# Optimization experiments

Hardware: AMD Instinct MI355X
Metric: run time of the kernel (lower is better)

The kernel has to match this reference:

```python
import math
import jax, jax.numpy as jnp
import numpy as np
from jax import lax

B, H, W, C1, D, NH = 32, 28, 28, 64, 256, 8
KS, RATIO = 9, 0.0005
NEG = -1.0e9


def setup_inputs() -> dict:
    key = jax.random.key(0)
    ks = jax.random.split(key, 6)
    x = jax.random.normal(ks[0], (B, 1, H, W), jnp.float32)
    conv_w = jax.random.normal(ks[1], (C1, 1, KS, KS), jnp.float32) * 0.05
    channel_embed = jax.random.normal(ks[2], (C1, D), jnp.float32)
    in_proj_w = jax.random.normal(ks[3], (3 * D, D), jnp.float32) * (1.0 / math.sqrt(D))
    in_proj_b = jnp.zeros((3 * D,), jnp.float32)
    out_proj_w = jax.random.normal(ks[4], (D, D), jnp.float32) * (1.0 / math.sqrt(D))
    out_proj_b = jnp.zeros((D,), jnp.float32)
    return {"x": x, "conv_w": conv_w, "channel_embed": channel_embed,
            "in_proj_w": in_proj_w, "in_proj_b": in_proj_b,
            "out_proj_w": out_proj_w, "out_proj_b": out_proj_b}


def _pos_encoding_2d(h, w, dim):
    # even dims: sin(y * div), odd dims: cos(x * div)  (matches torch broadcast)
    div = jnp.exp(jnp.arange(0, dim, 2, dtype=jnp.float32) * (-math.log(10000.0) / dim))
    pe_even = jnp.sin(jnp.arange(h, dtype=jnp.float32)[:, None] * div)  # (h, dim/2)
    pe_odd = jnp.cos(jnp.arange(w, dtype=jnp.float32)[:, None] * div)   # (w, dim/2)
    pe = jnp.zeros((h, w, dim), jnp.float32)
    pe = pe.at[..., 0::2].set(jnp.broadcast_to(pe_even[:, None, :], (h, w, dim // 2)))
    pe = pe.at[..., 1::2].set(jnp.broadcast_to(pe_odd[None, :, :], (h, w, dim // 2)))
    return pe


def reference(x, conv_w, channel_embed, in_proj_w, in_proj_b, out_proj_w, out_proj_b):
    pad = KS // 2
    A = jax.nn.relu(lax.conv_general_dilated(
        x, conv_w, (1, 1), [(pad, pad), (pad, pad)],
        dimension_numbers=("NCHW", "OIHW", "NCHW")))  # (B, C1, H, W)

    # global top-k threshold (kthvalue equivalent)
    total = A.size
    k = max(1, int(math.ceil(RATIO * total)))
    if k >= total:
        mask_global = jnp.ones_like(A, dtype=bool)
    else:
        vals, _ = lax.top_k(A.reshape(-1), k)
        mask_global = A >= vals[-1]
    A_g = A * mask_global.astype(A.dtype)

    v = jnp.transpose(A_g, (0, 2, 3, 1))  # (B, H, W, C1)
    nz = v > 0
    count = nz.sum(axis=-1)  # (B, H, W)

    top2_vals, top2_idx = lax.top_k(v, 2)  # (B,H,W,2)
    cidx = jnp.arange(C1)
    sel2 = (cidx == top2_idx[..., 0:1]) | (cidx == top2_idx[..., 1:2])
    idx_single = jnp.argmax(jnp.where(nz, v, -jnp.inf), axis=-1)
    sel1 = cidx == idx_single[..., None]

    logits = jnp.where((count >= 2)[..., None] & sel2, v, NEG)
    logits = jnp.where((count == 1)[..., None] & sel1, v, logits)
    sparse_weights = jax.nn.softmax(logits, axis=-1)
    sparse_weights = jnp.where((count == 0)[..., None], 0.0, sparse_weights)

    loc_emb = jnp.einsum("bhwc,cd->bhwd", sparse_weights, channel_embed)
    loc_emb = loc_emb + _pos_encoding_2d(H, W, D)[None]
    seq = loc_emb.reshape(B, H * W, D)

    # torch nn.MultiheadAttention (batch_first, self-attn)
    qkv = seq @ in_proj_w.T + in_proj_b  # (B, S, 3D)
    q, kk, vv = jnp.split(qkv, 3, axis=-1)
    hd = D // NH
    def heads(t):
        return t.reshape(B, H * W, NH, hd).transpose(0, 2, 1, 3)  # (B, NH, S, hd)
    q, kk, vv = heads(q), heads(kk), heads(vv)
    scores = jnp.einsum("bnqd,bnkd->bnqk", q, kk) / math.sqrt(hd)
    attn = jax.nn.softmax(scores, axis=-1)
    ctx = jnp.einsum("bnqk,bnkd->bnqd", attn, vv)
    ctx = ctx.transpose(0, 2, 1, 3).reshape(B, H * W, D)
    attn_out = ctx @ out_proj_w.T + out_proj_b
    pooled = attn_out.mean(axis=1)  # (B, D)
    return pooled, sparse_weights, top2_idx
```

## Files before the change

### kernel.cpp

```cpp
#include <hip/hip_runtime.h>
#include <cmath>

#define NB 32
#define C1N 64
#define DIM 256
#define NHEAD 8
#define SEQL 784
#define NA 1605632
#define SEQN 6422528
#define KSEL 803u
#define QK2S (0.17677669529663687f * 1.4426950408889634f)
#define THR2 11.541560f
#define PECOEF (-0.03597789207803197f)

#define AS1 __attribute__((address_space(1)))
#define AS3 __attribute__((address_space(3)))

typedef __attribute__((ext_vector_type(8))) short bf16x8;
typedef __attribute__((ext_vector_type(4))) float f32x4;

__device__ __forceinline__ unsigned short f2b(float f) {
  unsigned u = __float_as_uint(f);
  unsigned r = u + 0x7fffu + ((u >> 16) & 1u);
  return (unsigned short)(r >> 16);
}

__device__ __forceinline__ unsigned cvt_pk_bf16(float lo, float hi) {
  unsigned r;
  asm("v_cvt_pk_bf16_f32 %0, %1, %2" : "=v"(r) : "v"(lo), "v"(hi));
  return r;
}

__global__ void k_zero(unsigned* __restrict__ p, int n) {
  int i = blockIdx.x * 256 + threadIdx.x;
  if (i < n) p[i] = 0u;
}

__global__ __launch_bounds__(256) void k_cast(const float* __restrict__ ipw,
                                              unsigned short* __restrict__ wb) {
  int i = blockIdx.x * 256 + threadIdx.x;
  wb[i] = f2b(ipw[i]);
}

__global__ __launch_bounds__(256) void k_conv(const float* __restrict__ x,
                                              const float* __restrict__ cw,
                                              float* __restrict__ vbuf) {
  __shared__ __align__(16) float ximg[1296];
  __shared__ float wlds[5184];
  int tid = threadIdx.x;
  int b = blockIdx.x / 7, sblk = blockIdx.x % 7;
  for (int e = tid; e < 1296; e += 256) ximg[e] = 0.f;
  for (int e = tid; e < 5184; e += 256) {
    int c = e / 81, t = e - c * 81;
    wlds[t * 64 + c] = cw[e];
  }
  __syncthreads();
  const float* xb = x + b * 784;
  for (int e = tid; e < 784; e += 256) {
    int row = e / 28, col = e - row * 28;
    ximg[(row + 4) * 36 + col + 4] = xb[e];
  }
  __syncthreads();
  int wv = tid >> 6, lane = tid & 63;
  for (int it = 0; it < 7; ++it) {
    int grp = sblk * 28 + it * 4 + wv;
    int hr = grp / 7, wc0 = (grp % 7) * 4;
    float a0 = 0.f, a1 = 0.f, a2 = 0.f, a3 = 0.f;
    #pragma unroll
    for (int dy = 0; dy < 9; ++dy) {
      const float4* xr4 = (const float4*)&ximg[(hr + dy) * 36 + wc0];
      float4 xa = xr4[0], xbq = xr4[1], xc = xr4[2];
      float xr[12] = {xa.x, xa.y, xa.z, xa.w, xbq.x, xbq.y, xbq.z, xbq.w,
                      xc.x, xc.y, xc.z, xc.w};
      #pragma unroll
      for (int dx = 0; dx < 9; ++dx) {
        float w = wlds[(dy * 9 + dx) * 64 + lane];
        a0 = fmaf(xr[dx + 0], w, a0);
        a1 = fmaf(xr[dx + 1], w, a1);
        a2 = fmaf(xr[dx + 2], w, a2);
        a3 = fmaf(xr[dx + 3], w, a3);
      }
    }
    size_t base = ((size_t)(b * 784 + hr * 28 + wc0)) * 64 + lane;
    vbuf[base +   0] = fmaxf(a0, 0.f);
    vbuf[base +  64] = fmaxf(a1, 0.f);
    vbuf[base + 128] = fmaxf(a2, 0.f);
    vbuf[base + 192] = fmaxf(a3, 0.f);
  }
}

__global__ __launch_bounds__(256) void k_h8(const float* __restrict__ vbuf,
                                            const unsigned* __restrict__ sel,
                                            unsigned* __restrict__ hist8,
                                            int stage) {
  __shared__ unsigned lh[256];
  int tid = threadIdx.x;
  lh[tid] = 0u;
  __syncthreads();
  if (stage == 0 || sel[2] == 0u) {
    unsigned key = (stage == 1) ? sel[0] : 0u;
    const float4* v4 = (const float4*)vbuf;
    int n4 = NA / 4;
    for (int i = blockIdx.x * 256 + tid; i < n4; i += gridDim.x * 256) {
      float4 v = v4[i];
      float vv[4] = {v.x, v.y, v.z, v.w};
      #pragma unroll
      for (int j = 0; j < 4; ++j) {
        if (vv[j] > 0.0f) {
          unsigned bits = __float_as_uint(vv[j]);
          if (stage == 0) atomicAdd(&lh[bits >> 24], 1u);
          else if ((bits >> 24) == key) atomicAdd(&lh[(bits >> 16) & 0xFFu], 1u);
        }
      }
    }
  }
  __syncthreads();
  if (lh[tid] > 0u) atomicAdd(&hist8[tid], lh[tid]);
}

__global__ __launch_bounds__(256) void k_scan8(const unsigned* __restrict__ hist8,
                                               unsigned* __restrict__ sel,
                                               int stage) {
  if (stage == 1 && sel[2]) return;
  __shared__ unsigned ss[256];
  int t = threadIdx.x;
  ss[t] = hist8[t];
  __syncthreads();
  for (int off = 1; off < 256; off <<= 1) {
    unsigned v = (t + off < 256) ? ss[t + off] : 0u;
    __syncthreads();
    ss[t] += v;
    __syncthreads();
  }
  unsigned rem = (stage == 0) ? KSEL : sel[1];
  if (stage == 0 && t == 0 && ss[0] < KSEL) {
    sel[2] = 1u; sel[3] = 0u;
  }
  unsigned S = ss[t];
  unsigned above = (t < 255) ? ss[t + 1] : 0u;
  if (S >= rem && above < rem) {
    if (stage == 0) { sel[0] = (unsigned)t; sel[1] = rem - above; }
    else            { sel[4] = (unsigned)t; sel[5] = rem - above; }
  }
}

__global__ __launch_bounds__(256) void k_h16(const float* __restrict__ vbuf,
                                             const unsigned* __restrict__ sel,
                                             unsigned* __restrict__ hist16) {
  if (sel[2]) return;
  unsigned key16 = (sel[0] << 8) | sel[4];
  const float4* v4 = (const float4*)vbuf;
  int n4 = NA / 4;
  for (int i = blockIdx.x * 256 + threadIdx.x; i < n4; i += gridDim.x * 256) {
    float4 v = v4[i];
    float vv[4] = {v.x, v.y, v.z, v.w};
    #pragma unroll
    for (int j = 0; j < 4; ++j) {
      if (vv[j] > 0.0f) {
        unsigned bits = __float_as_uint(vv[j]);
        if ((bits >> 16) == key16) atomicAdd(&hist16[bits & 0xFFFFu], 1u);
      }
    }
  }
}

__global__ __launch_bounds__(1024) void k_scan16(const unsigned* __restrict__ hist16,
                                                 unsigned* __restrict__ sel) {
  if (sel[2]) return;
  __shared__ unsigned ss[1024];
  int t = threadIdx.x;
  unsigned rem = sel[5];
  unsigned sum = 0;
  for (int i = 0; i < 64; ++i) sum += hist16[t * 64 + i];
  ss[t] = sum;
  __syncthreads();
  for (int off = 1; off < 1024; off <<= 1) {
    unsigned v = (t + off < 1024) ? ss[t + off] : 0u;
    __syncthreads();
    ss[t] += v;
    __syncthreads();
  }
  unsigned S = ss[t];
  unsigned above = (t < 1023) ? ss[t + 1] : 0u;
  if (S >= rem && above < rem) {
    unsigned cum = above;
    for (int bb = t * 64 + 63; bb >= t * 64; --bb) {
      unsigned hb = hist16[bb];
      cum += hb;
      if (cum >= rem) {
        sel[3] = (((sel[0] << 8) | sel[4]) << 16) | (unsigned)bb;
        break;
      }
    }
  }
}

__global__ __launch_bounds__(256) void k_select(const float* __restrict__ vbuf,
                                                const unsigned* __restrict__ sel,
                                                const float* __restrict__ ce,
                                                unsigned short* __restrict__ seqb,
                                                float* __restrict__ out_sw,
                                                float* __restrict__ out_idx) {
  int wid = threadIdx.x >> 6;
  int lane = threadIdx.x & 63;
  int pos = blockIdx.x * 4 + wid;
  int hw = pos % 784;
  int hr = hw / 28;
  int wc = hw % 28;
  float thr = __uint_as_float(sel[3]);
  float a = vbuf[(size_t)pos * 64 + lane];
  float val = (a >= thr) ? a : 0.0f;
  unsigned long long nzm = __ballot(val > 0.0f);
  int count = __popcll(nzm);
  float v1 = val; int i1 = lane;
  #pragma unroll
  for (int off = 32; off > 0; off >>= 1) {
    float ov = __shfl_xor(v1, off);
    int oi = __shfl_xor(i1, off);
    if (ov > v1 || (ov == v1 && oi < i1)) { v1 = ov; i1 = oi; }
  }
  float vx = (lane == i1) ? -INFINITY : val;
  float v2 = vx; int i2 = lane;
  #pragma unroll
  for (int off = 32; off > 0; off >>= 1) {
    float ov = __shfl_xor(v2, off);
    int oi = __shfl_xor(i2, off);
    if (ov > v2 || (ov == v2 && oi < i2)) { v2 = ov; i2 = oi; }
  }
  float w1 = 0.0f, w2 = 0.0f;
  if (count >= 2) {
    float e = __expf(v2 - v1);
    float invd = 1.0f / (1.0f + e);
    w1 = invd; w2 = e * invd;
  } else if (count == 1) {
    w1 = 1.0f;
  }
  float wt = (lane == i1) ? w1 : ((lane == i2) ? w2 : 0.0f);
  out_sw[(size_t)pos * 64 + lane] = wt;
  if (lane < 2) out_idx[pos * 2 + lane] = (float)(lane == 0 ? i1 : i2);
  int d0 = lane * 4;
  float4 c1v = *(const float4*)(ce + (size_t)i1 * 256 + d0);
  float4 c2v = *(const float4*)(ce + (size_t)i2 * 256 + d0);
  float dv0 = __expf((float)d0 * PECOEF);
  float dv2 = __expf((float)(d0 + 2) * PECOEF);
  float ox = w1 * c1v.x + w2 * c2v.x + __sinf((float)hr * dv0);
  float oy = w1 * c1v.y + w2 * c2v.y + __cosf((float)wc * dv0);
  float oz = w1 * c1v.z + w2 * c2v.z + __sinf((float)hr * dv2);
  float ow = w1 * c1v.w + w2 * c2v.w + __cosf((float)wc * dv2);
  ushort4 ob = make_ushort4(f2b(ox), f2b(oy), f2b(oz), f2b(ow));
  *(ushort4*)(seqb + (size_t)pos * 256 + d0) = ob;
}

__global__ __launch_bounds__(256) void k_gemm_lds(const unsigned short* __restrict__ A,
                                                  const unsigned short* __restrict__ W,
                                                  const float* __restrict__ bias,
                                                  unsigned short* __restrict__ C,
                                                  int M, int N, int K) {
  __shared__ __align__(16) unsigned short As[8192];
  __shared__ __align__(16) unsigned short Bs[8192];
  int tid = threadIdx.x;
  int lane = tid & 63, wid = tid >> 6;
  int q = lane & 15, g = lane >> 4;
  int m0 = blockIdx.y * 128, n0 = blockIdx.x * 128;
  int lrow = lane >> 3, s = lane & 7;
  const unsigned short* aSrc = A + (size_t)(m0 + wid * 8 + lrow) * K + (s ^ lrow) * 8;
  const unsigned short* bSrc = W + (size_t)(n0 + wid * 8 + lrow) * K + (s ^ lrow) * 8;
  int dstW = wid * 512;
  int mloc = (wid >> 1) * 64, nloc = (wid & 1) * 64;
  int q7 = q & 7;
  f32x4 acc[4][4];
  #pragma unroll
  for (int i = 0; i < 4; ++i)
    #pragma unroll
    for (int j = 0; j < 4; ++j) acc[i][j] = (f32x4){0.f, 0.f, 0.f, 0.f};
  for (int k0 = 0; k0 < K; k0 += 64) {
    #pragma unroll
    for (int i = 0; i < 4; ++i) {
      __builtin_amdgcn_global_load_lds((const AS1 void*)(aSrc + (size_t)i * 32 * K + k0),
                                       (AS3 void*)(&As[i * 2048 + dstW]), 16, 0, 0);
      __builtin_amdgcn_global_load_lds((const AS1 void*)(bSrc + (size_t)i * 32 * K + k0),
                                       (AS3 void*)(&Bs[i * 2048 + dstW]), 16, 0, 0);
    }
    __syncthreads();
    #pragma unroll
    for (int kk = 0; kk < 2; ++kk) {
      bf16x8 af[4], bf[4];
      #pragma unroll
      for (int i = 0; i < 4; ++i)
        af[i] = *(const bf16x8*)&As[(mloc + i * 16 + q) * 64 + (((kk * 4 + g) ^ q7) * 8)];
      #pragma unroll
      for (int j = 0; j < 4; ++j)
        bf[j] = *(const bf16x8*)&Bs[(nloc + j * 16 + q) * 64 + (((kk * 4 + g) ^ q7) * 8)];
      __builtin_amdgcn_s_setprio(1);
      #pragma unroll
      for (int i = 0; i < 4; ++i)
        #pragma unroll
        for (int j = 0; j < 4; ++j)
          acc[i][j] = __builtin_amdgcn_mfma_f32_16x16x32_bf16(af[i], bf[j], acc[i][j], 0, 0, 0);
      __builtin_amdgcn_s_setprio(0);
    }
    __syncthreads();
  }
  #pragma unroll
  for (int j = 0; j < 4; ++j) {
    int col = n0 + nloc + j * 16 + q;
    float bj = bias[col];
    float qs = (col < 256) ? QK2S : 1.0f;
    #pragma unroll
    for (int i = 0; i < 4; ++i) {
      #pragma unroll
      for (int r = 0; r < 4; ++r) {
        int row = m0 + mloc + i * 16 + g * 4 + r;
        C[(size_t)row * N + col] = f2b((acc[i][j][r] + bj) * qs);
      }
    }
  }
}

__global__ __launch_bounds__(256) void k_vt(const unsigned short* __restrict__ qkv,
                                            unsigned short* __restrict__ Vt) {
  __shared__ unsigned short lds[32][72];
  int k0 = blockIdx.x * 64;
  int bh = blockIdx.y;
  int b = bh >> 3, nh = bh & 7;
  int tid = threadIdx.x;
  int key = tid >> 2;
  int c8 = (tid & 3) * 8;
  int kk = k0 + key;
  ushort4 a = make_ushort4(0, 0, 0, 0), bq = a;
  if (kk < 784) {
    const unsigned short* src = qkv + (size_t)(b * 784 + kk) * 768 + 512 + nh * 32 + c8;
    a  = *(const ushort4*)src;
    bq = *(const ushort4*)(src + 4);
  }
  lds[c8 + 0][key] = a.x;  lds[c8 + 1][key] = a.y;
  lds[c8 + 2][key] = a.z;  lds[c8 + 3][key] = a.w;
  lds[c8 + 4][key] = bq.x; lds[c8 + 5][key] = bq.y;
  lds[c8 + 6][key] = bq.z; lds[c8 + 7][key] = bq.w;
  __syncthreads();
  int d = tid >> 3;
  int kc = (tid & 7) * 8;
  if (k0 + kc < 800) {
    int sb = (kc & 32) + ((kc >> 3) & 3) * 4;
    ushort4 o0 = make_ushort4(lds[d][sb + 0],  lds[d][sb + 1],
                              lds[d][sb + 2],  lds[d][sb + 3]);
    ushort4 o1 = make_ushort4(lds[d][sb + 16], lds[d][sb + 17],
                              lds[d][sb + 18], lds[d][sb + 19]);
    unsigned short* dst = Vt + ((size_t)bh * 32 + d) * 800 + k0 + kc;
    *(ushort4*)dst = o0;
    *(ushort4*)(dst + 4) = o1;
  }
}

__global__ __launch_bounds__(256) void k_attn(const unsigned short* __restrict__ qkv,
                                              const unsigned short* __restrict__ Vt,
                                              unsigned short* __restrict__ ctx) {
  __shared__ __align__(16) unsigned short Kt[2][1024];
  __shared__ __align__(16) unsigned short Vti[2][1024];
  int wid = threadIdx.x >> 6;
  int lane = threadIdx.x & 63;
  int blk = blockIdx.x;
  int wb = (blk & 7) * 416 + (blk >> 3);
  int bh = wb / 13;
  int qb = (wb - bh * 13) * 4 + wid;
  int b = bh >> 3, nh = bh & 7;
  int q = lane & 15, g = lane >> 4;
  bool active = (qb < 49);
  const f32x4 zero4 = {0.f, 0.f, 0.f, 0.f};

  int qrow = b * 784 + (active ? qb * 16 + q : q);
  bf16x8 qf = *(const bf16x8*)(qkv + (size_t)qrow * 768 + nh * 32 + g * 8);
  const unsigned short* kbase = qkv + (size_t)b * 784 * 768 + 256 + nh * 32;
  const unsigned short* vbase = Vt + (size_t)bh * 32 * 800;

  int rit = ((wid & 1) << 4) + (lane >> 2);
  int sG = (lane & 3) ^ ((rit + (rit >> 2)) & 3);
  bool isK = (wid < 2);
  int ldsoff = ((wid & 1) << 4) * 32;

  int slotr = ((g ^ ((q + (q >> 2)) & 3)) << 3);
  int rowA = q * 32 + slotr;
  int rowB = (16 + q) * 32 + slotr;

  f32x4 acc0 = zero4, acc1 = zero4;
  float m = -INFINITY, lp = 0.f;

#define STAGE(buf, k0v)                                                         \
  {                                                                             \
    if (isK) {                                                                  \
      int key_ = (k0v) + rit; if (key_ > 783) key_ = 783;                       \
      __builtin_amdgcn_global_load_lds(                                         \
        (const AS1 void*)(kbase + (size_t)key_ * 768 + sG * 8),                 \
        (AS3 void*)(&Kt[buf][ldsoff]), 16, 0, 0);                               \
    } else {                                                                    \
      __builtin_amdgcn_global_load_lds(                                         \
        (const AS1 void*)(vbase + (size_t)rit * 800 + (k0v) + sG * 8),          \
        (AS3 void*)(&Vti[buf][ldsoff]), 16, 0, 0);                              \
    }                                                                           \
  }

  STAGE(0, 0);
  __syncthreads();

  for (int c = 0; c < 24; ++c) {
    int cur = c & 1;
    STAGE(cur ^ 1, (c + 1) * 32);
    bf16x8 kA = *(const bf16x8*)&Kt[cur][rowA];
    bf16x8 kB = *(const bf16x8*)&Kt[cur][rowB];
    bf16x8 va = *(const bf16x8*)&Vti[cur][rowA];
    bf16x8 vb = *(const bf16x8*)&Vti[cur][rowB];
    __builtin_amdgcn_s_setprio(1);
    f32x4 s0 = __builtin_amdgcn_mfma_f32_16x16x32_bf16(kA, qf, zero4, 0, 0, 0);
    f32x4 s1 = __builtin_amdgcn_mfma_f32_16x16x32_bf16(kB, qf, zero4, 0, 0, 0);
    __builtin_amdgcn_s_setprio(0);
    float pl = fmaxf(fmaxf(fmaxf(s0[0], s0[1]), fmaxf(s0[2], s0[3])),
                     fmaxf(fmaxf(s1[0], s1[1]), fmaxf(s1[2], s1[3])));
    if (!__all(pl <= m + THR2)) {
      float pm = fmaxf(pl, __shfl_xor(pl, 16));
      pm = fmaxf(pm, __shfl_xor(pm, 32));
      float mnew = fmaxf(m, pm);
      float sc = __builtin_amdgcn_exp2f(m - mnew);
      lp *= sc; acc0 *= sc; acc1 *= sc;
      m = mnew;
    }
    float p0[4], p1[4];
    #pragma unroll
    for (int r = 0; r < 4; ++r) {
      p0[r] = __builtin_amdgcn_exp2f(s0[r] - m);
      p1[r] = __builtin_amdgcn_exp2f(s1[r] - m);
    }
    lp += ((p0[0] + p0[1]) + (p0[2] + p0[3])) + ((p1[0] + p1[1]) + (p1[2] + p1[3]));
    union { unsigned u[4]; bf16x8 v; } pu;
    pu.u[0] = cvt_pk_bf16(p0[0], p0[1]);
    pu.u[1] = cvt_pk_bf16(p0[2], p0[3]);
    pu.u[2] = cvt_pk_bf16(p1[0], p1[1]);
    pu.u[3] = cvt_pk_bf16(p1[2], p1[3]);
    __builtin_amdgcn_s_setprio(1);
    acc0 = __builtin_amdgcn_mfma_f32_16x16x32_bf16(va, pu.v, acc0, 0, 0, 0);
    acc1 = __builtin_amdgcn_mfma_f32_16x16x32_bf16(vb, pu.v, acc1, 0, 0, 0);
    __builtin_amdgcn_s_setprio(0);
    __syncthreads();
  }
  {
    bf16x8 kA = *(const bf16x8*)&Kt[0][rowA];
    bf16x8 va = *(const bf16x8*)&Vti[0][rowA];
    bf16x8 vb = *(const bf16x8*)&Vti[0][rowB];
    f32x4 s0 = __builtin_amdgcn_mfma_f32_16x16x32_bf16(kA, qf, zero4, 0, 0, 0);
    float pl = fmaxf(fmaxf(s0[0], s0[1]), fmaxf(s0[2], s0[3]));
    if (!__all(pl <= m + THR2)) {
      float pm = fmaxf(pl, __shfl_xor(pl, 16));
      pm = fmaxf(pm, __shfl_xor(pm, 32));
      float mnew = fmaxf(m, pm);
      float sc = __builtin_amdgcn_exp2f(m - mnew);
      lp *= sc; acc0 *= sc; acc1 *= sc;
      m = mnew;
    }
    float p0[4];
    #pragma unroll
    for (int r = 0; r < 4; ++r) p0[r] = __builtin_amdgcn_exp2f(s0[r] - m);
    lp += (p0[0] + p0[1]) + (p0[2] + p0[3]);
    union { unsigned u[4]; bf16x8 v; } pu;
    pu.u[0] = cvt_pk_bf16(p0[0], p0[1]);
    pu.u[1] = cvt_pk_bf16(p0[2], p0[3]);
    pu.u[2] = 0u;
    pu.u[3] = 0u;
    acc0 = __builtin_amdgcn_mfma_f32_16x16x32_bf16(va, pu.v, acc0, 0, 0, 0);
    acc1 = __builtin_amdgcn_mfma_f32_16x16x32_bf16(vb, pu.v, acc1, 0, 0, 0);
  }
#undef STAGE
  float l = lp + __shfl_xor(lp, 16);
  l += __shfl_xor(l, 32);
  float linv = 1.f / l;
  if (active) {
    unsigned short* cp = ctx + (size_t)(b * 784 + qb * 16 + q) * 256 + nh * 32;
    ushort4 oA = make_ushort4(f2b(acc0[0] * linv), f2b(acc0[1] * linv),
                              f2b(acc0[2] * linv), f2b(acc0[3] * linv));
    ushort4 oB = make_ushort4(f2b(acc1[0] * linv), f2b(acc1[1] * linv),
                              f2b(acc1[2] * linv), f2b(acc1[3] * linv));
    *(ushort4*)(cp + g * 4) = oA;
    *(ushort4*)(cp + 16 + g * 4) = oB;
  }
}

__global__ __launch_bounds__(256) void k_poolctx(const unsigned short* __restrict__ ctx,
                                                 float* __restrict__ part) {
  int b = blockIdx.x >> 3, sseg = blockIdx.x & 7;
  int d = threadIdx.x;
  const unsigned short* base = ctx + ((size_t)b * 784 + sseg * 98) * 256 + d;
  float acc = 0.f;
  for (int t = 0; t < 98; ++t)
    acc += __uint_as_float((unsigned)base[(size_t)t * 256] << 16);
  part[(size_t)blockIdx.x * 256 + d] = acc;
}

__global__ __launch_bounds__(256) void k_pgemv(const float* __restrict__ part,
                                               const float* __restrict__ opw,
                                               const float* __restrict__ opb,
                                               float* __restrict__ out) {
  __shared__ float mc[256];
  int b = blockIdx.x, d = threadIdx.x;
  float s = 0.f;
  #pragma unroll
  for (int i = 0; i < 8; ++i) s += part[(size_t)(b * 8 + i) * 256 + d];
  mc[d] = s * (1.0f / 784.0f);
  __syncthreads();
  float acc = opb[d];
  const float4* wr = (const float4*)(opw + (size_t)d * 256);
  #pragma unroll 8
  for (int j = 0; j < 64; ++j) {
    float4 w = wr[j];
    float4 m4 = *(const float4*)&mc[j * 4];
    acc += m4.x * w.x + m4.y * w.y + m4.z * w.z + m4.w * w.w;
  }
  out[b * 256 + d] = acc;
}

extern "C" void kernel_launch(void* const* d_in, const int* in_sizes, int n_in,
                              void* d_out, int out_size, void* d_ws, size_t ws_size,
                              hipStream_t stream) {
  (void)in_sizes; (void)n_in; (void)out_size; (void)ws_size;
  const float* x   = (const float*)d_in[0];
  const float* cw  = (const float*)d_in[1];
  const float* ce  = (const float*)d_in[2];
  const float* ipw = (const float*)d_in[3];
  const float* ipb = (const float*)d_in[4];
  const float* opw = (const float*)d_in[5];
  const float* opb = (const float*)d_in[6];

  float* out = (float*)d_out;
  float* pooled  = out;
  float* out_sw  = out + 8192;
  float* out_idx = out + 8192 + NA;

  float* ws = (float*)d_ws;
  float* vbuf = ws;
  unsigned* hist16 = (unsigned*)(ws + NA);
  unsigned* hist8a = hist16 + 65536;
  unsigned* hist8b = hist8a + 256;
  unsigned* sel    = hist8b + 256;
  unsigned short* seqb = (unsigned short*)(ws + NA + 66080);
  unsigned short* qkvb = seqb + SEQN;
  unsigned short* Vt   = qkvb + 3 * (size_t)SEQN;
  unsigned short* wb   = Vt + 256 * 32 * 800;
  float* part = (float*)(wb + 262144);

  k_zero<<<(66080 + 255) / 256, 256, 0, stream>>>(hist16, 66080);
  k_cast<<<768, 256, 0, stream>>>(ipw, wb);
  k_conv<<<224, 256, 0, stream>>>(x, cw, vbuf);
  k_h8<<<1024, 256, 0, stream>>>(vbuf, sel, hist8a, 0);
  k_scan8<<<1, 256, 0, stream>>>(hist8a, sel, 0);
  k_h8<<<1024, 256, 0, stream>>>(vbuf, sel, hist8b, 1);
  k_scan8<<<1, 256, 0, stream>>>(hist8b, sel, 1);
  k_h16<<<1024, 256, 0, stream>>>(vbuf, sel, hist16);
  k_scan16<<<1, 1024, 0, stream>>>(hist16, sel);
  k_select<<<25088 / 4, 256, 0, stream>>>(vbuf, sel, ce, seqb, out_sw, out_idx);
  {
    dim3 gq(768 / 128, 25088 / 128);
    k_gemm_lds<<<gq, 256, 0, stream>>>(seqb, wb, ipb, qkvb, 25088, 768, 256);
  }
  {
    dim3 gv(13, 256);
    k_vt<<<gv, 256, 0, stream>>>(qkvb, Vt);
  }
  k_attn<<<3328, 256, 0, stream>>>(qkvb, Vt, seqb );
  k_poolctx<<<256, 256, 0, stream>>>(seqb, part);
  k_pgemv<<<NB, 256, 0, stream>>>(part, opw, opb, pooled);
}
```

Baseline: 191.1 us.

## Triple-buffer attention K/V staging with vmcnt waits and merge init kernels

```diff
diff --git a/kernel.cpp b/kernel.cpp
--- a/kernel.cpp
+++ b/kernel.cpp
@@ -31,15 +31,12 @@
   return r;
 }
 
-__global__ void k_zero(unsigned* __restrict__ p, int n) {
+__global__ __launch_bounds__(256) void k_init(const float* __restrict__ ipw,
+                                              unsigned short* __restrict__ wbuf,
+                                              unsigned* __restrict__ z) {
   int i = blockIdx.x * 256 + threadIdx.x;
-  if (i < n) p[i] = 0u;
-}
-
-__global__ __launch_bounds__(256) void k_cast(const float* __restrict__ ipw,
-                                              unsigned short* __restrict__ wb) {
-  int i = blockIdx.x * 256 + threadIdx.x;
-  wb[i] = f2b(ipw[i]);
+  if (i < 66080) z[i] = 0u;
+  wbuf[i] = f2b(ipw[i]);
 }
 
 __global__ __launch_bounds__(256) void k_conv(const float* __restrict__ x,
@@ -355,14 +352,14 @@
 __global__ __launch_bounds__(256) void k_attn(const unsigned short* __restrict__ qkv,
                                               const unsigned short* __restrict__ Vt,
                                               unsigned short* __restrict__ ctx) {
-  __shared__ __align__(16) unsigned short Kt[2][1024];
-  __shared__ __align__(16) unsigned short Vti[2][1024];
+  __shared__ __align__(16) unsigned short Kt[3][1024];
+  __shared__ __align__(16) unsigned short Vti[3][1024];
   int wid = threadIdx.x >> 6;
   int lane = threadIdx.x & 63;
   int blk = blockIdx.x;
-  int wb = (blk & 7) * 416 + (blk >> 3);
-  int bh = wb / 13;
-  int qb = (wb - bh * 13) * 4 + wid;
+  int wrk = (blk & 7) * 416 + (blk >> 3);
+  int bh = wrk / 13;
+  int qb = (wrk - bh * 13) * 4 + wid;
   int b = bh >> 3, nh = bh & 7;
   int q = lane & 15, g = lane >> 4;
   bool active = (qb < 49);
@@ -370,6 +367,8 @@
 
   int qrow = b * 784 + (active ? qb * 16 + q : q);
   bf16x8 qf = *(const bf16x8*)(qkv + (size_t)qrow * 768 + nh * 32 + g * 8);
+  asm volatile("s_waitcnt vmcnt(0)" ::: "memory");
+
   const unsigned short* kbase = qkv + (size_t)b * 784 * 768 + 256 + nh * 32;
   const unsigned short* vbase = Vt + (size_t)bh * 32 * 800;
 
@@ -377,6 +376,10 @@
   int sG = (lane & 3) ^ ((rit + (rit >> 2)) & 3);
   bool isK = (wid < 2);
   int ldsoff = ((wid & 1) << 4) * 32;
+  const unsigned short* sp = isK ? (kbase + (size_t)rit * 768 + sG * 8)
+                                 : (vbase + (size_t)rit * 800 + sG * 8);
+  const int sstride = isK ? (32 * 768) : 32;
+  unsigned short* ldsb = (isK ? &Kt[0][0] : &Vti[0][0]) + ldsoff;
 
   int slotr = ((g ^ ((q + (q >> 2)) & 3)) << 3);
   int rowA = q * 32 + slotr;
@@ -385,63 +388,65 @@
   f32x4 acc0 = zero4, acc1 = zero4;
   float m = -INFINITY, lp = 0.f;
 
-#define STAGE(buf, k0v)                                                         \
-  {                                                                             \
-    if (isK) {                                                                  \
-      int key_ = (k0v) + rit; if (key_ > 783) key_ = 783;                       \
-      __builtin_amdgcn_global_load_lds(                                         \
-        (const AS1 void*)(kbase + (size_t)key_ * 768 + sG * 8),                 \
-        (AS3 void*)(&Kt[buf][ldsoff]), 16, 0, 0);                               \
-    } else {                                                                    \
-      __builtin_amdgcn_global_load_lds(                                         \
-        (const AS1 void*)(vbase + (size_t)rit * 800 + (k0v) + sG * 8),          \
-        (AS3 void*)(&Vti[buf][ldsoff]), 16, 0, 0);                              \
-    }                                                                           \
-  }
-
-  STAGE(0, 0);
-  __syncthreads();
-
-  for (int c = 0; c < 24; ++c) {
-    int cur = c & 1;
-    STAGE(cur ^ 1, (c + 1) * 32);
-    bf16x8 kA = *(const bf16x8*)&Kt[cur][rowA];
-    bf16x8 kB = *(const bf16x8*)&Kt[cur][rowB];
-    bf16x8 va = *(const bf16x8*)&Vti[cur][rowA];
-    bf16x8 vb = *(const bf16x8*)&Vti[cur][rowB];
-    __builtin_amdgcn_s_setprio(1);
-    f32x4 s0 = __builtin_amdgcn_mfma_f32_16x16x32_bf16(kA, qf, zero4, 0, 0, 0);
-    f32x4 s1 = __builtin_amdgcn_mfma_f32_16x16x32_bf16(kB, qf, zero4, 0, 0, 0);
-    __builtin_amdgcn_s_setprio(0);
-    float pl = fmaxf(fmaxf(fmaxf(s0[0], s0[1]), fmaxf(s0[2], s0[3])),
-                     fmaxf(fmaxf(s1[0], s1[1]), fmaxf(s1[2], s1[3])));
-    if (!__all(pl <= m + THR2)) {
-      float pm = fmaxf(pl, __shfl_xor(pl, 16));
-      pm = fmaxf(pm, __shfl_xor(pm, 32));
-      float mnew = fmaxf(m, pm);
-      float sc = __builtin_amdgcn_exp2f(m - mnew);
-      lp *= sc; acc0 *= sc; acc1 *= sc;
-      m = mnew;
-    }
-    float p0[4], p1[4];
-    #pragma unroll
-    for (int r = 0; r < 4; ++r) {
-      p0[r] = __builtin_amdgcn_exp2f(s0[r] - m);
-      p1[r] = __builtin_amdgcn_exp2f(s1[r] - m);
-    }
-    lp += ((p0[0] + p0[1]) + (p0[2] + p0[3])) + ((p1[0] + p1[1]) + (p1[2] + p1[3]));
-    union { unsigned u[4]; bf16x8 v; } pu;
-    pu.u[0] = cvt_pk_bf16(p0[0], p0[1]);
-    pu.u[1] = cvt_pk_bf16(p0[2], p0[3]);
-    pu.u[2] = cvt_pk_bf16(p1[0], p1[1]);
-    pu.u[3] = cvt_pk_bf16(p1[2], p1[3]);
-    __builtin_amdgcn_s_setprio(1);
-    acc0 = __builtin_amdgcn_mfma_f32_16x16x32_bf16(va, pu.v, acc0, 0, 0, 0);
-    acc1 = __builtin_amdgcn_mfma_f32_16x16x32_bf16(vb, pu.v, acc1, 0, 0, 0);
-    __builtin_amdgcn_s_setprio(0);
-    __syncthreads();
+#define STAGE(BUFO) {                                                          \
+    __builtin_amdgcn_global_load_lds((const AS1 void*)sp,                      \
+                                     (AS3 void*)(ldsb + (BUFO)), 16, 0, 0);    \
+    sp += sstride; }
+
+#define STEP(CUR, NXT) {                                                       \
+    asm volatile("s_waitcnt vmcnt(1)" ::: "memory");                           \
+    __builtin_amdgcn_s_barrier();                                              \
+    asm volatile("" ::: "memory");                                             \
+    STAGE(NXT);                                                                \
+    bf16x8 kA = *(const bf16x8*)&Kt[0][(CUR) + rowA];                          \
+    bf16x8 kB = *(const bf16x8*)&Kt[0][(CUR) + rowB];                          \
+    bf16x8 va = *(const bf16x8*)&Vti[0][(CUR) + rowA];                         \
+    bf16x8 vb = *(const bf16x8*)&Vti[0][(CUR) + rowB];                         \
+    __builtin_amdgcn_s_setprio(1);                                             \
+    f32x4 s0 = __builtin_amdgcn_mfma_f32_16x16x32_bf16(kA, qf, zero4, 0, 0, 0);\
+    f32x4 s1 = __builtin_amdgcn_mfma_f32_16x16x32_bf16(kB, qf, zero4, 0, 0, 0);\
+    __builtin_amdgcn_s_setprio(0);                                             \
+    float pl = fmaxf(fmaxf(fmaxf(s0[0], s0[1]), fmaxf(s0[2], s0[3])),          \
+                     fmaxf(fmaxf(s1[0], s1[1]), fmaxf(s1[2], s1[3])));         \
+    if (!__all(pl <= m + THR2)) {                                              \
+      float pm = fmaxf(pl, __shfl_xor(pl, 16));                                \
+      pm = fmaxf(pm, __shfl_xor(pm, 32));                                      \
+      float mnew = fmaxf(m, pm);                                               \
+      float sc = __builtin_amdgcn_exp2f(m - mnew);                             \
+      lp *= sc; acc0 *= sc; acc1 *= sc;                                        \
+      m = mnew;                                                                \
+    }                                                                          \
+    float p0[4], p1[4];                                                        \
+    _Pragma("unroll")                                                          \
+    for (int r = 0; r < 4; ++r) {                                              \
+      p0[r] = __builtin_amdgcn_exp2f(s0[r] - m);                               \
+      p1[r] = __builtin_amdgcn_exp2f(s1[r] - m);                               \
+    }                                                                          \
+    lp += ((p0[0] + p0[1]) + (p0[2] + p0[3]))                                  \
+        + ((p1[0] + p1[1]) + (p1[2] + p1[3]));                                 \
+    union { unsigned u[4]; bf16x8 v; } pu;                                     \
+    pu.u[0] = cvt_pk_bf16(p0[0], p0[1]);                                       \
+    pu.u[1] = cvt_pk_bf16(p0[2], p0[3]);                                       \
+    pu.u[2] = cvt_pk_bf16(p1[0], p1[1]);                                       \
+    pu.u[3] = cvt_pk_bf16(p1[2], p1[3]);                                       \
+    __builtin_amdgcn_s_setprio(1);                                             \
+    acc0 = __builtin_amdgcn_mfma_f32_16x16x32_bf16(va, pu.v, acc0, 0, 0, 0);   \
+    acc1 = __builtin_amdgcn_mfma_f32_16x16x32_bf16(vb, pu.v, acc1, 0, 0, 0);   \
+    __builtin_amdgcn_s_setprio(0);                                             \
+  }
+
+  STAGE(0);
+  STAGE(1024);
+
+  for (int t = 0; t < 8; ++t) {
+    STEP(0, 2048);
+    STEP(1024, 0);
+    STEP(2048, 1024);
   }
   {
+    asm volatile("s_waitcnt vmcnt(1)" ::: "memory");
+    __builtin_amdgcn_s_barrier();
+    asm volatile("" ::: "memory");
     bf16x8 kA = *(const bf16x8*)&Kt[0][rowA];
     bf16x8 va = *(const bf16x8*)&Vti[0][rowA];
     bf16x8 vb = *(const bf16x8*)&Vti[0][rowB];
@@ -467,6 +472,7 @@
     acc0 = __builtin_amdgcn_mfma_f32_16x16x32_bf16(va, pu.v, acc0, 0, 0, 0);
     acc1 = __builtin_amdgcn_mfma_f32_16x16x32_bf16(vb, pu.v, acc1, 0, 0, 0);
   }
+#undef STEP
 #undef STAGE
   float l = lp + __shfl_xor(lp, 16);
   l += __shfl_xor(l, 32);
@@ -541,11 +547,10 @@
   unsigned short* seqb = (unsigned short*)(ws + NA + 66080);
   unsigned short* qkvb = seqb + SEQN;
   unsigned short* Vt   = qkvb + 3 * (size_t)SEQN;
-  unsigned short* wb   = Vt + 256 * 32 * 800;
-  float* part = (float*)(wb + 262144);
-
-  k_zero<<<(66080 + 255) / 256, 256, 0, stream>>>(hist16, 66080);
-  k_cast<<<768, 256, 0, stream>>>(ipw, wb);
+  unsigned short* wbuf = Vt + 256 * 32 * 800;
+  float* part = (float*)(wbuf + 262144);
+
+  k_init<<<768, 256, 0, stream>>>(ipw, wbuf, hist16);
   k_conv<<<224, 256, 0, stream>>>(x, cw, vbuf);
   k_h8<<<1024, 256, 0, stream>>>(vbuf, sel, hist8a, 0);
   k_scan8<<<1, 256, 0, stream>>>(hist8a, sel, 0);
@@ -556,7 +561,7 @@
   k_select<<<25088 / 4, 256, 0, stream>>>(vbuf, sel, ce, seqb, out_sw, out_idx);
   {
     dim3 gq(768 / 128, 25088 / 128);
-    k_gemm_lds<<<gq, 256, 0, stream>>>(seqb, wb, ipb, qkvb, 25088, 768, 256);
+    k_gemm_lds<<<gq, 256, 0, stream>>>(seqb, wbuf, ipb, qkvb, 25088, 768, 256);
   }
   {
     dim3 gv(13, 256);
```

Result: faster. 183.2 us (-4.1%).
